# Performance work log

Hardware: AMD Instinct MI355X
Metric: run time of the kernel (lower is better)

## Reference

```python
import jax, jax.numpy as jnp
import numpy as np

EPS = 1e-6
H = 16       # query heads
KVH = 8      # kv heads
DH = 64      # head dim
HID = 1024


def _rms_norm(x, w, eps=EPS):
    ms = jnp.mean(jnp.square(x.astype(jnp.float32)), axis=-1, keepdims=True) + eps
    y = x.astype(jnp.float32) * jax.lax.rsqrt(ms)
    if w is not None:
        y = y * w.astype(jnp.float32)
    return y.astype(x.dtype)


def _rotate_half(x):
    h = x.shape[-1] // 2
    return jnp.concatenate([-x[..., h:], x[..., :h]], axis=-1)


def _multi_axis_rope(x, cos, sin, ndim):
    # x: [B,S,Hd,DH]; cos/sin: [S, rot_total]
    dh = x.shape[-1]
    rot = 2 * (dh // (2 * ndim))
    outs = []
    for i in range(ndim):
        sl = slice(i * rot, (i + 1) * rot)
        xp = x[..., sl]
        cp = cos[:, sl][:, None, :]   # [S,1,rot] broadcasts over heads
        sp = sin[:, sl][:, None, :]
        outs.append(xp * cp + _rotate_half(xp) * sp)
    return jnp.concatenate(outs, axis=-1)


def setup_inputs() -> dict:
    key = jax.random.key(0)
    ks = jax.random.split(key, 10)
    B, S = 4, 2048
    inp = {
        "hidden_states": jax.random.normal(ks[0], (B, S, HID), dtype=jnp.float32),
        "cos": jax.random.uniform(ks[1], (S, DH), dtype=jnp.float32, minval=-1.0, maxval=1.0),
        "sin": jax.random.uniform(ks[2], (S, DH), dtype=jnp.float32, minval=-1.0, maxval=1.0),
        "position_ids": jax.random.randint(ks[3], (B, S, 2), 0, 64).astype(jnp.int64),
        "attention_mask": jnp.ones((B, S), dtype=bool),
        "Wq": jax.random.normal(ks[4], (HID, H * DH), dtype=jnp.float32) * 0.02,
        "Wk": jax.random.normal(ks[5], (HID, KVH * DH), dtype=jnp.float32) * 0.02,
        "Wv": jax.random.normal(ks[6], (HID, KVH * DH), dtype=jnp.float32) * 0.02,
        "Wo": jax.random.normal(ks[7], (H * DH, HID), dtype=jnp.float32) * 0.02,
        "q_norm_w": jnp.ones((DH,), dtype=jnp.float32),
        "k_norm_w": jnp.ones((DH,), dtype=jnp.float32),
    }
    return inp


def reference(hidden_states, cos, sin, position_ids, attention_mask, Wq, Wk, Wv, Wo, q_norm_w, k_norm_w):
    B, S, _ = hidden_states.shape
    ndim = int(position_ids.shape[-1])

    q = (hidden_states @ Wq).reshape(B, S, H, DH)
    k = (hidden_states @ Wk).reshape(B, S, KVH, DH)
    v = (hidden_states @ Wv).reshape(B, S, KVH, DH)

    q = _rms_norm(q, q_norm_w)
    k = _rms_norm(k, k_norm_w)
    v = _rms_norm(v, None)  # v_norm has no scale

    q = _multi_axis_rope(q, cos, sin, ndim)
    k = _multi_axis_rope(k, cos, sin, ndim)

    # [B, heads, S, DH]; repeat kv heads for GQA
    q = q.transpose(0, 2, 1, 3)
    k = jnp.repeat(k.transpose(0, 2, 1, 3), H // KVH, axis=1)
    v = jnp.repeat(v.transpose(0, 2, 1, 3), H // KVH, axis=1)

    scores = jnp.einsum("bhqd,bhkd->bhqk", q, k)  # scaling = 1.0
    key_mask = attention_mask[:, None, None, :]
    scores = jnp.where(key_mask, scores, jnp.finfo(scores.dtype).min)
    probs = jax.nn.softmax(scores.astype(jnp.float32), axis=-1).astype(v.dtype)

    out = jnp.einsum("bhqk,bhkd->bhqd", probs, v)
    out = out.transpose(0, 2, 1, 3).reshape(B, S, H * DH)
    out = jnp.where(attention_mask[:, :, None], out, 0.0)
    return out @ Wo
```

## Files before the change

kernel.cpp:

```cpp
#include <hip/hip_runtime.h>
#include <stdint.h>
#include <stddef.h>

typedef unsigned short u16;
typedef unsigned int   u32;
typedef unsigned short u16x8 __attribute__((ext_vector_type(8)));
typedef __attribute__((ext_vector_type(8))) __bf16 bf16x8;
typedef __attribute__((ext_vector_type(4))) float f32x4;

__device__ __forceinline__ float bf2f(u16 v){
  union { unsigned u; float f; } x; x.u = ((unsigned)v) << 16; return x.f;
}
__device__ __forceinline__ u16 f2bf(float f){
  union { float f; unsigned u; } x; x.f = f;
  return (u16)((x.u + 0x7fffu + ((x.u >> 16) & 1u)) >> 16);
}

__device__ __forceinline__ float exp2_fast(float x){
  float r; asm("v_exp_f32 %0, %1" : "=v"(r) : "v"(x)); return r;
}
__device__ __forceinline__ u32 cvt_pk_bf16(float lo, float hi){
  u32 r; asm("v_cvt_pk_bf16_f32 %0, %1, %2" : "=v"(r) : "v"(lo), "v"(hi)); return r;
}

__device__ __forceinline__ f32x4 mfma16(bf16x8 a, bf16x8 b, f32x4 c){
  return __builtin_amdgcn_mfma_f32_16x16x32_bf16(a, b, c, 0, 0, 0);
}

#define AS1 __attribute__((address_space(1)))
#define AS3 __attribute__((address_space(3)))
__device__ __forceinline__ void gload_lds16(const void* g, void* l){
  __builtin_amdgcn_global_load_lds((const AS1 void*)g, (AS3 void*)l, 16, 0, 0);
}

__global__ void f32_to_bf16_swz(const float* __restrict__ in, u16* __restrict__ out,
                                int total_chunks){
  for (int i = blockIdx.x * blockDim.x + threadIdx.x; i < total_chunks;
       i += gridDim.x * blockDim.x){
    int row = i >> 7, c = i & 127;
    int cs = (c & ~7) | ((c & 7) ^ (row & 7));
    const float* p = in + ((size_t)i << 3);
    float4 v0 = *(const float4*)p;
    float4 v1 = *(const float4*)(p + 4);
    u16x8 o = { f2bf(v0.x), f2bf(v0.y), f2bf(v0.z), f2bf(v0.w),
                f2bf(v1.x), f2bf(v1.y), f2bf(v1.z), f2bf(v1.w) };
    *(u16x8*)(out + (((size_t)row << 7) + cs) * 8) = o;
  }
}

__global__ void conv_transpose_swz(const float* __restrict__ in, u16* __restrict__ out,
                                   int R, int C){
  __shared__ float t[32][33];
  int c0 = blockIdx.x * 32, r0 = blockIdx.y * 32;
  int tx = threadIdx.x, ty = threadIdx.y;
  t[ty][tx] = in[(size_t)(r0 + ty) * C + c0 + tx];
  __syncthreads();
  int tid = ty * 32 + tx;
  if (tid < 128){
    int orow = tid >> 2, oc = tid & 3;
    int gr = c0 + orow;
    int gc = (r0 >> 3) + oc;
    int gcs = (gc & ~7) | ((gc & 7) ^ (gr & 7));
    u16x8 v;
#pragma unroll
    for (int i = 0; i < 8; i++) v[i] = f2bf(t[oc * 8 + i][orow]);
    *(u16x8*)(out + (size_t)gr * R + gcs * 8) = v;
  }
}

template<int BM, int WM, bool F32OUT>
__global__ __launch_bounds__(512, 2)
void gemm256(const u16* __restrict__ A, const u16* __restrict__ Bt,
             void* __restrict__ Cv, int M, int N, int K){
  constexpr int MF = WM / 16;
  constexpr int ALOADS = BM / 64;
  __shared__ __align__(16) u16 Ab[3][BM * 64];
  const int tid = threadIdx.x;
  const int wid = tid >> 6, lane = tid & 63;
  const int g = lane >> 4, col = lane & 15;
  const int wm = wid >> 2, wn = wid & 3;
  const int swz = col & 7;

  int nb  = gridDim.x * gridDim.y;
  int lid = blockIdx.y * gridDim.x + blockIdx.x;
  int cpx = nb >> 3;
  int sid = (lid & 7) * cpx + (lid >> 3);
  int bx  = sid % gridDim.x, by = sid / gridDim.x;
  const int m0 = by * BM, n0 = bx * 256;

  f32x4 acc[MF][4];
#pragma unroll
  for (int i = 0; i < MF; i++)
#pragma unroll
    for (int j = 0; j < 4; j++) acc[i][j] = (f32x4){0.f, 0.f, 0.f, 0.f};

  const int arow = wid * 8 + (lane >> 3);
  const int acl  = (lane & 7) * 8;

  auto STAGE_A = [&](int bi, int k0){
#pragma unroll
    for (int j = 0; j < ALOADS; j++)
      gload_lds16(A + (size_t)(m0 + j * 64 + arow) * K + k0 + acl,
                  &Ab[bi][j * 4096 + wid * 512]);
  };

  const int NT = K >> 6;
  STAGE_A(0, 0);
  STAGE_A(1, 64);
  if (ALOADS == 4) asm volatile("s_waitcnt vmcnt(4)");
  else             asm volatile("s_waitcnt vmcnt(2)");
  __builtin_amdgcn_sched_barrier(0);
  __builtin_amdgcn_s_barrier();
  __builtin_amdgcn_sched_barrier(0);

  int cb = 0, sa = 2;
  for (int t = 0; t < NT; ++t){
    bf16x8 bfr[4][2];
#pragma unroll
    for (int ni = 0; ni < 4; ni++){
      const u16* bp = Bt + (size_t)(n0 + wn * 64 + ni * 16 + col) * K + t * 64;
#pragma unroll
      for (int ks = 0; ks < 2; ks++)
        bfr[ni][ks] = *(const bf16x8*)(bp + (((ks * 4 + g) ^ swz) << 3));
    }
    __builtin_amdgcn_sched_barrier(0);
    if (t + 2 < NT) STAGE_A(sa, (t + 2) * 64);
    __builtin_amdgcn_sched_barrier(0);

    const u16* Ac = &Ab[cb][0];
#pragma unroll
    for (int ph = 0; ph < MF / 4; ++ph){
      bf16x8 afr[4][2];
#pragma unroll
      for (int m2 = 0; m2 < 4; m2++){
        int row = wm * WM + (ph * 4 + m2) * 16 + col;
#pragma unroll
        for (int ks = 0; ks < 2; ks++)
          afr[m2][ks] = *(const bf16x8*)&Ac[row * 64 + (((ks * 4 + g) ^ swz) << 3)];
      }
      __builtin_amdgcn_s_setprio(1);
#pragma unroll
      for (int m2 = 0; m2 < 4; m2++)
#pragma unroll
        for (int ni = 0; ni < 4; ni++)
#pragma unroll
          for (int ks = 0; ks < 2; ks++)
            acc[ph * 4 + m2][ni] =
                mfma16(afr[m2][ks], bfr[ni][ks], acc[ph * 4 + m2][ni]);
      __builtin_amdgcn_s_setprio(0);
    }

    asm volatile("s_waitcnt lgkmcnt(0)");
    __builtin_amdgcn_sched_barrier(0);
    if (t + 2 < NT){
      if (ALOADS == 4) asm volatile("s_waitcnt vmcnt(4)");
      else             asm volatile("s_waitcnt vmcnt(2)");
    } else {
      asm volatile("s_waitcnt vmcnt(0)");
    }
    __builtin_amdgcn_sched_barrier(0);
    __builtin_amdgcn_s_barrier();
    __builtin_amdgcn_sched_barrier(0);
    cb = (cb == 2) ? 0 : cb + 1;
    sa = (sa == 2) ? 0 : sa + 1;
  }

#pragma unroll
  for (int mi = 0; mi < MF; mi++)
#pragma unroll
    for (int ni = 0; ni < 4; ni++)
#pragma unroll
      for (int r = 0; r < 4; r++){
        int row = m0 + wm * WM + mi * 16 + g * 4 + r;
        int cc  = n0 + wn * 64 + ni * 16 + col;
        if (F32OUT) ((float*)Cv)[(size_t)row * N + cc] = acc[mi][ni][r];
        else        ((u16*)Cv)[(size_t)row * N + cc] = f2bf(acc[mi][ni][r]);
      }
}

__global__ void prep_q(const u16* __restrict__ qkv, u16* __restrict__ Qn,
                       const float* __restrict__ cosb, const float* __restrict__ sinb,
                       const float* __restrict__ w){
  int gid = blockIdx.x * 4 + (threadIdx.x >> 6);
  int lane = threadIdx.x & 63;
  int s = gid & 2047;
  int bh = gid >> 11;
  int h = bh & 15, b = bh >> 4;
  float x = bf2f(qkv[((size_t)(b * 2048 + s)) * 2048 + h * 64 + lane]);
  float ss = x * x;
#pragma unroll
  for (int off = 32; off >= 1; off >>= 1) ss += __shfl_xor(ss, off, 64);
  float y = x * rsqrtf(ss * (1.f / 64.f) + 1e-6f);
  y *= w[lane];
  float yp = __shfl_xor(y, 16, 64);
  float rot = (lane & 16) ? yp : -yp;
  Qn[(size_t)gid * 64 + lane] = f2bf(y * cosb[s * 64 + lane] + rot * sinb[s * 64 + lane]);
}

__global__ void prep_k(const u16* __restrict__ qkv, u16* __restrict__ Kn,
                       const float* __restrict__ cosb, const float* __restrict__ sinb,
                       const float* __restrict__ w){
  int gid = blockIdx.x * 4 + (threadIdx.x >> 6);
  int lane = threadIdx.x & 63;
  int s = gid & 2047;
  int bk = gid >> 11;
  int kvh = bk & 7, b = bk >> 3;
  float x = bf2f(qkv[((size_t)(b * 2048 + s)) * 2048 + 1024 + kvh * 64 + lane]);
  float ss = x * x;
#pragma unroll
  for (int off = 32; off >= 1; off >>= 1) ss += __shfl_xor(ss, off, 64);
  float y = x * rsqrtf(ss * (1.f / 64.f) + 1e-6f);
  y *= w[lane];
  float yp = __shfl_xor(y, 16, 64);
  float rot = (lane & 16) ? yp : -yp;
  int swz = ((((lane >> 3) ^ s) & 7) << 3) | (lane & 7);
  Kn[(size_t)gid * 64 + swz] = f2bf(y * cosb[s * 64 + lane] + rot * sinb[s * 64 + lane]);
}

__global__ __launch_bounds__(256)
void prep_v(const u16* __restrict__ qkv, u16* __restrict__ Vn){
  int blk = blockIdx.x;
  int stile = blk & 31, kvh = (blk >> 5) & 7, b = blk >> 8;
  int wid = threadIdx.x >> 6, lane = threadIdx.x & 63;
  __shared__ u16 T[64][68];
#pragma unroll 4
  for (int j = 0; j < 16; j++){
    int sl = wid * 16 + j;
    int s = stile * 64 + sl;
    float x = bf2f(qkv[((size_t)(b * 2048 + s)) * 2048 + 1536 + kvh * 64 + lane]);
    float ss = x * x;
#pragma unroll
    for (int off = 32; off >= 1; off >>= 1) ss += __shfl_xor(ss, off, 64);
    T[sl][lane] = f2bf(x * rsqrtf(ss * (1.f / 64.f) + 1e-6f));
  }
  __syncthreads();
  size_t obase = ((size_t)(b * 8 + kvh) * 64) * 2048 + stile * 64;
#pragma unroll
  for (int it = 0; it < 2; it++){
    int t = it * 256 + threadIdx.x;
    int d = t >> 3, c = t & 7;
    int cl = c ^ (d & 7);
    u16x8 v;
#pragma unroll
    for (int i = 0; i < 8; i++) v[i] = T[cl * 8 + i][d];
    *(u16x8*)(Vn + obase + (size_t)d * 2048 + c * 8) = v;
  }
}

__global__ __launch_bounds__(256, 2)
void flash_attn(const u16* __restrict__ Qn, const u16* __restrict__ Kn,
                const u16* __restrict__ Vn, u16* __restrict__ AO){
  const int S = 2048;
  const float L2E = 1.4426950408889634f;
  const float C2 = 30.f;
  const int b = blockIdx.z, h = blockIdx.y, qt = blockIdx.x;
  const int kvh = h >> 1;
  const int wid = threadIdx.x >> 6, lane = threadIdx.x & 63;
  const int g = lane >> 4, col = lane & 15;
  const int q0 = qt * 256 + wid * 64;

  __shared__ __align__(16) u16 Klds[2][64 * 64];
  __shared__ __align__(16) u16 Vlds[2][64 * 64];
  __shared__ __align__(16) u16 Plds[4][16 * 64];

  bf16x8 ones;
#pragma unroll
  for (int i = 0; i < 8; i++) ones[i] = (__bf16)1.0f;

  bf16x8 aq[4][2];
#pragma unroll
  for (int cg = 0; cg < 4; cg++){
    const u16* qp = Qn + ((size_t)((b * 16 + h) * S) + q0 + cg * 16 + col) * 64;
    aq[cg][0] = *(const bf16x8*)(qp + g * 8);
    aq[cg][1] = *(const bf16x8*)(qp + 32 + g * 8);
  }

  const u16* Kbase = Kn + (size_t)(b * 8 + kvh) * S * 64;
  const u16* Vbase = Vn + (size_t)(b * 8 + kvh) * 64 * S;

  f32x4 acc[4][4];
  f32x4 lacc[4];
#pragma unroll
  for (int cg = 0; cg < 4; cg++){
    lacc[cg] = (f32x4){0.f, 0.f, 0.f, 0.f};
#pragma unroll
    for (int i = 0; i < 4; i++) acc[cg][i] = (f32x4){0.f, 0.f, 0.f, 0.f};
  }

  const int sw = col & 7;
  const int pswz = sw << 4;
  char* Pw = (char*)&Plds[wid][0];

  auto STAGE = [&](int bi, int kt){
    int kc0 = kt * 64;
#pragma unroll
    for (int cc = 0; cc < 2; cc++){
      int chunk = cc * 4 + wid;
      gload_lds16(Kbase + (size_t)kc0 * 64 + chunk * 512 + lane * 8,
                  &Klds[bi][chunk * 512]);
      int drow = chunk * 8 + (lane >> 3);
      gload_lds16(Vbase + (size_t)drow * S + kc0 + (lane & 7) * 8,
                  &Vlds[bi][chunk * 512]);
    }
  };

  int buf = 0;
  STAGE(0, 0);
  __syncthreads();

  for (int kt = 0; kt < S / 64; ++kt){
    if (kt + 1 < S / 64) STAGE(buf ^ 1, kt + 1);

    const u16* Kb = &Klds[buf][0];
    const u16* Vb = &Vlds[buf][0];

    bf16x8 kf[4][2], vf[4][2];
#pragma unroll
    for (int c = 0; c < 4; c++){
      const u16* kb = Kb + (c * 16 + col) * 64;
      kf[c][0] = *(const bf16x8*)(kb + (g ^ sw) * 8);
      kf[c][1] = *(const bf16x8*)(kb + ((4 + g) ^ sw) * 8);
      const u16* vb = Vb + (c * 16 + col) * 64;
      vf[c][0] = *(const bf16x8*)(vb + (g ^ sw) * 8);
      vf[c][1] = *(const bf16x8*)(vb + ((4 + g) ^ sw) * 8);
    }

#pragma unroll
    for (int cg = 0; cg < 4; cg++){
      f32x4 sf[4];
      __builtin_amdgcn_s_setprio(1);
#pragma unroll
      for (int c = 0; c < 4; c++){
        f32x4 z = (f32x4){0.f, 0.f, 0.f, 0.f};
        z = mfma16(kf[c][0], aq[cg][0], z);
        sf[c] = mfma16(kf[c][1], aq[cg][1], z);
      }
      __builtin_amdgcn_s_setprio(0);

#pragma unroll
      for (int c = 0; c < 4; c++){
        float p0 = exp2_fast(__builtin_fmaf(sf[c][0], L2E, -C2));
        float p1 = exp2_fast(__builtin_fmaf(sf[c][1], L2E, -C2));
        float p2 = exp2_fast(__builtin_fmaf(sf[c][2], L2E, -C2));
        float p3 = exp2_fast(__builtin_fmaf(sf[c][3], L2E, -C2));
        uint2 pw;
        pw.x = cvt_pk_bf16(p0, p1);
        pw.y = cvt_pk_bf16(p2, p3);
        *(uint2*)(Pw + ((col * 128 + c * 32 + g * 8) ^ pswz)) = pw;
      }

      bf16x8 pf0 = *(const bf16x8*)(Pw + ((col * 128 + g * 16) ^ pswz));
      bf16x8 pf1 = *(const bf16x8*)(Pw + ((col * 128 + 64 + g * 16) ^ pswz));
      __builtin_amdgcn_s_setprio(1);
#pragma unroll
      for (int cd = 0; cd < 4; cd++){
        acc[cg][cd] = mfma16(vf[cd][0], pf0, acc[cg][cd]);
        acc[cg][cd] = mfma16(vf[cd][1], pf1, acc[cg][cd]);
      }
      lacc[cg] = mfma16(ones, pf0, lacc[cg]);
      lacc[cg] = mfma16(ones, pf1, lacc[cg]);
      __builtin_amdgcn_s_setprio(0);
    }

    __syncthreads();
    buf ^= 1;
  }

#pragma unroll
  for (int cg = 0; cg < 4; cg++){
    float linv = 1.f / lacc[cg][0];
    int s = q0 + cg * 16 + col;
#pragma unroll
    for (int cd = 0; cd < 4; cd++){
      uint2 o;
      o.x = cvt_pk_bf16(acc[cg][cd][0] * linv, acc[cg][cd][1] * linv);
      o.y = cvt_pk_bf16(acc[cg][cd][2] * linv, acc[cg][cd][3] * linv);
      int pc = (cd * 2 + (g >> 1)) ^ sw;
      *(uint2*)(AO + (size_t)(b * S + s) * 1024 + h * 64 + pc * 8 + (g & 1) * 4) = o;
    }
  }
}

extern "C" void kernel_launch(void* const* d_in, const int* in_sizes, int n_in,
                              void* d_out, int out_size, void* d_ws, size_t ws_size,
                              hipStream_t stream){
  const int Btok = 8192;
  const float* hs   = (const float*)d_in[0];
  const float* cosb = (const float*)d_in[1];
  const float* sinb = (const float*)d_in[2];
  const float* Wq = (const float*)d_in[5];
  const float* Wk = (const float*)d_in[6];
  const float* Wv = (const float*)d_in[7];
  const float* Wo = (const float*)d_in[8];
  const float* qw = (const float*)d_in[9];
  const float* kw = (const float*)d_in[10];
  float* out = (float*)d_out;

  char* ws = (char*)d_ws;
  u16* hsB   = (u16*)ws;               ws += (size_t)Btok * 1024 * 2;
  u16* WqkvT = (u16*)ws;               ws += (size_t)2048 * 1024 * 2;
  u16* WoT   = (u16*)ws;               ws += (size_t)1024 * 1024 * 2;
  u16* QKV   = (u16*)ws;               ws += (size_t)Btok * 2048 * 2;
  u16* Qn    = (u16*)ws;               ws += (size_t)Btok * 1024 * 2;
  u16* Kn    = (u16*)ws;               ws += (size_t)Btok * 512  * 2;
  u16* Vn    = (u16*)ws;               ws += (size_t)Btok * 512  * 2;
  u16* AO    = hsB;

  f32_to_bf16_swz<<<2048, 256, 0, stream>>>(hs, hsB, Btok * 128);

  dim3 tb(32, 32);
  conv_transpose_swz<<<dim3(32, 32), tb, 0, stream>>>(Wq, WqkvT,               1024, 1024);
  conv_transpose_swz<<<dim3(16, 32), tb, 0, stream>>>(Wk, WqkvT + 1024 * 1024, 1024, 512);
  conv_transpose_swz<<<dim3(16, 32), tb, 0, stream>>>(Wv, WqkvT + 1536 * 1024, 1024, 512);
  conv_transpose_swz<<<dim3(32, 32), tb, 0, stream>>>(Wo, WoT,                 1024, 1024);

  gemm256<256, 128, false><<<dim3(8, 32), 512, 0, stream>>>(hsB, WqkvT, QKV, Btok, 2048, 1024);

  prep_q<<<32768, 256, 0, stream>>>(QKV, Qn, cosb, sinb, qw);
  prep_k<<<16384, 256, 0, stream>>>(QKV, Kn, cosb, sinb, kw);
  prep_v<<<1024, 256, 0, stream>>>(QKV, Vn);

  flash_attn<<<dim3(8, 16, 4), 256, 0, stream>>>(Qn, Kn, Vn, AO);

  gemm256<128, 64, true><<<dim3(4, 64), 512, 0, stream>>>(AO, WoT, out, Btok, 1024, 1024);
}
```

Baseline: 205.2 us.

## Fuse QKV RMSNorm, RoPE and layout into QKV GEMM epilogue

The separate prep_q, prep_k and prep_v kernels are removed. The QKV GEMM epilogue now computes per-row RMS norm with lane shuffles, applies the weights and RoPE from a packed cos/sin table, and writes Q, K (swizzled) and transposed V directly. This avoids writing and re-reading the intermediate QKV buffer and saves three launches. In exchange, the GEMM epilogue gains extra register pressure and uses scattered 2-byte stores for Q and K.

```diff
diff --git a/kernel.cpp b/kernel.cpp
--- a/kernel.cpp
+++ b/kernel.cpp
@@ -68,10 +68,19 @@
   }
 }
 
-template<int BM, int WM, bool F32OUT>
+__global__ void pack_cs(const float* __restrict__ cosb, const float* __restrict__ sinb,
+                        float2* __restrict__ cs, int n){
+  int i = blockIdx.x * 256 + threadIdx.x;
+  if (i < n) cs[i] = (float2){cosb[i], sinb[i]};
+}
+
+template<int BM, int WM, int EPI>
 __global__ __launch_bounds__(512, 2)
 void gemm256(const u16* __restrict__ A, const u16* __restrict__ Bt,
-             void* __restrict__ Cv, int M, int N, int K){
+             void* __restrict__ Cv, int M, int N, int K,
+             const float2* __restrict__ cs, const float* __restrict__ qw,
+             const float* __restrict__ kw, u16* __restrict__ Qn,
+             u16* __restrict__ Kn, u16* __restrict__ Vn){
   constexpr int MF = WM / 16;
   constexpr int ALOADS = BM / 64;
   __shared__ __align__(16) u16 Ab[3][BM * 64];
@@ -165,6 +174,92 @@
     sa = (sa == 2) ? 0 : sa + 1;
   }
 
+  if (EPI == 1){
+    const int colbase = n0 + wn * 64;
+    const int t0 = m0 + wm * WM;
+    const int bb = t0 >> 11;
+    if (colbase < 1536){
+      const bool isQ = colbase < 1024;
+      const int head = isQ ? (colbase >> 6) : ((colbase - 1024) >> 6);
+      const float* wp = isQ ? qw : kw;
+      float wv[4];
+#pragma unroll
+      for (int ni = 0; ni < 4; ni++) wv[ni] = wp[ni * 16 + col];
+      u16* outp = isQ ? Qn : Kn;
+      size_t hb = isQ ? ((size_t)(bb * 16 + head) * 2048)
+                      : ((size_t)(bb * 8 + head) * 2048);
+#pragma unroll
+      for (int mi = 0; mi < MF; mi++){
+        f32x4 ssv = (f32x4){0.f, 0.f, 0.f, 0.f};
+#pragma unroll
+        for (int ni = 0; ni < 4; ni++)
+#pragma unroll
+          for (int r = 0; r < 4; r++) ssv[r] += acc[mi][ni][r] * acc[mi][ni][r];
+#pragma unroll
+        for (int off = 1; off < 16; off <<= 1)
+#pragma unroll
+          for (int r = 0; r < 4; r++) ssv[r] += __shfl_xor(ssv[r], off, 64);
+        f32x4 rinv;
+#pragma unroll
+        for (int r = 0; r < 4; r++) rinv[r] = rsqrtf(ssv[r] * (1.f / 64.f) + 1e-6f);
+        int s0 = (t0 + mi * 16 + g * 4) & 2047;
+#pragma unroll
+        for (int np = 0; np < 2; np++){
+          int d0 = np * 32 + col, d1 = d0 + 16;
+#pragma unroll
+          for (int r = 0; r < 4; r++){
+            int s = s0 + r;
+            float y0 = acc[mi][np * 2][r]     * rinv[r] * wv[np * 2];
+            float y1 = acc[mi][np * 2 + 1][r] * rinv[r] * wv[np * 2 + 1];
+            float2 c0 = cs[s * 64 + d0];
+            float2 c1 = cs[s * 64 + d1];
+            float o0 = y0 * c0.x - y1 * c0.y;
+            float o1 = y1 * c1.x + y0 * c1.y;
+            if (isQ){
+              outp[(hb + s) * 64 + d0] = f2bf(o0);
+              outp[(hb + s) * 64 + d1] = f2bf(o1);
+            } else {
+              int z0 = ((((d0 >> 3) ^ s) & 7) << 3) | (d0 & 7);
+              int z1 = ((((d1 >> 3) ^ s) & 7) << 3) | (d1 & 7);
+              outp[(hb + s) * 64 + z0] = f2bf(o0);
+              outp[(hb + s) * 64 + z1] = f2bf(o1);
+            }
+          }
+        }
+      }
+    } else {
+      const int kvh = (colbase - 1536) >> 6;
+      const size_t vb0 = (size_t)(bb * 8 + kvh) * 64;
+#pragma unroll
+      for (int mi = 0; mi < MF; mi++){
+        f32x4 ssv = (f32x4){0.f, 0.f, 0.f, 0.f};
+#pragma unroll
+        for (int ni = 0; ni < 4; ni++)
+#pragma unroll
+          for (int r = 0; r < 4; r++) ssv[r] += acc[mi][ni][r] * acc[mi][ni][r];
+#pragma unroll
+        for (int off = 1; off < 16; off <<= 1)
+#pragma unroll
+          for (int r = 0; r < 4; r++) ssv[r] += __shfl_xor(ssv[r], off, 64);
+        f32x4 rinv;
+#pragma unroll
+        for (int r = 0; r < 4; r++) rinv[r] = rsqrtf(ssv[r] * (1.f / 64.f) + 1e-6f);
+        int s0 = (t0 + mi * 16 + g * 4) & 2047;
+#pragma unroll
+        for (int ni = 0; ni < 4; ni++){
+          int d = ni * 16 + col;
+          uint2 o;
+          o.x = cvt_pk_bf16(acc[mi][ni][0] * rinv[0], acc[mi][ni][1] * rinv[1]);
+          o.y = cvt_pk_bf16(acc[mi][ni][2] * rinv[2], acc[mi][ni][3] * rinv[3]);
+          size_t addr = (vb0 + d) * 2048 + (s0 & ~63)
+                      + ((((s0 >> 3) ^ (d & 7)) & 7) << 3) + (s0 & 7);
+          *(uint2*)(Vn + addr) = o;
+        }
+      }
+    }
+    return;
+  }
+
 #pragma unroll
   for (int mi = 0; mi < MF; mi++)
 #pragma unroll
@@ -173,78 +268,9 @@
       for (int r = 0; r < 4; r++){
         int row = m0 + wm * WM + mi * 16 + g * 4 + r;
         int cc  = n0 + wn * 64 + ni * 16 + col;
-        if (F32OUT) ((float*)Cv)[(size_t)row * N + cc] = acc[mi][ni][r];
-        else        ((u16*)Cv)[(size_t)row * N + cc] = f2bf(acc[mi][ni][r]);
-      }
-}
-
-__global__ void prep_q(const u16* __restrict__ qkv, u16* __restrict__ Qn,
-                       const float* __restrict__ cosb, const float* __restrict__ sinb,
-                       const float* __restrict__ w){
-  int gid = blockIdx.x * 4 + (threadIdx.x >> 6);
-  int lane = threadIdx.x & 63;
-  int s = gid & 2047;
-  int bh = gid >> 11;
-  int h = bh & 15, b = bh >> 4;
-  float x = bf2f(qkv[((size_t)(b * 2048 + s)) * 2048 + h * 64 + lane]);
-  float ss = x * x;
-#pragma unroll
-  for (int off = 32; off >= 1; off >>= 1) ss += __shfl_xor(ss, off, 64);
-  float y = x * rsqrtf(ss * (1.f / 64.f) + 1e-6f);
-  y *= w[lane];
-  float yp = __shfl_xor(y, 16, 64);
-  float rot = (lane & 16) ? yp : -yp;
-  Qn[(size_t)gid * 64 + lane] = f2bf(y * cosb[s * 64 + lane] + rot * sinb[s * 64 + lane]);
-}
-
-__global__ void prep_k(const u16* __restrict__ qkv, u16* __restrict__ Kn,
-                       const float* __restrict__ cosb, const float* __restrict__ sinb,
-                       const float* __restrict__ w){
-  int gid = blockIdx.x * 4 + (threadIdx.x >> 6);
-  int lane = threadIdx.x & 63;
-  int s = gid & 2047;
-  int bk = gid >> 11;
-  int kvh = bk & 7, b = bk >> 3;
-  float x = bf2f(qkv[((size_t)(b * 2048 + s)) * 2048 + 1024 + kvh * 64 + lane]);
-  float ss = x * x;
-#pragma unroll
-  for (int off = 32; off >= 1; off >>= 1) ss += __shfl_xor(ss, off, 64);
-  float y = x * rsqrtf(ss * (1.f / 64.f) + 1e-6f);
-  y *= w[lane];
-  float yp = __shfl_xor(y, 16, 64);
-  float rot = (lane & 16) ? yp : -yp;
-  int swz = ((((lane >> 3) ^ s) & 7) << 3) | (lane & 7);
-  Kn[(size_t)gid * 64 + swz] = f2bf(y * cosb[s * 64 + lane] + rot * sinb[s * 64 + lane]);
-}
-
-__global__ __launch_bounds__(256)
-void prep_v(const u16* __restrict__ qkv, u16* __restrict__ Vn){
-  int blk = blockIdx.x;
-  int stile = blk & 31, kvh = (blk >> 5) & 7, b = blk >> 8;
-  int wid = threadIdx.x >> 6, lane = threadIdx.x & 63;
-  __shared__ u16 T[64][68];
-#pragma unroll 4
-  for (int j = 0; j < 16; j++){
-    int sl = wid * 16 + j;
-    int s = stile * 64 + sl;
-    float x = bf2f(qkv[((size_t)(b * 2048 + s)) * 2048 + 1536 + kvh * 64 + lane]);
-    float ss = x * x;
-#pragma unroll
-    for (int off = 32; off >= 1; off >>= 1) ss += __shfl_xor(ss, off, 64);
-    T[sl][lane] = f2bf(x * rsqrtf(ss * (1.f / 64.f) + 1e-6f));
-  }
-  __syncthreads();
-  size_t obase = ((size_t)(b * 8 + kvh) * 64) * 2048 + stile * 64;
-#pragma unroll
-  for (int it = 0; it < 2; it++){
-    int t = it * 256 + threadIdx.x;
-    int d = t >> 3, c = t & 7;
-    int cl = c ^ (d & 7);
-    u16x8 v;
-#pragma unroll
-    for (int i = 0; i < 8; i++) v[i] = T[cl * 8 + i][d];
-    *(u16x8*)(Vn + obase + (size_t)d * 2048 + c * 8) = v;
-  }
+        if (EPI == 2) ((float*)Cv)[(size_t)row * N + cc] = acc[mi][ni][r];
+        else          ((u16*)Cv)[(size_t)row * N + cc] = f2bf(acc[mi][ni][r]);
+      }
 }
 
 __global__ __launch_bounds__(256, 2)
@@ -400,10 +426,10 @@
   u16* hsB   = (u16*)ws;               ws += (size_t)Btok * 1024 * 2;
   u16* WqkvT = (u16*)ws;               ws += (size_t)2048 * 1024 * 2;
   u16* WoT   = (u16*)ws;               ws += (size_t)1024 * 1024 * 2;
-  u16* QKV   = (u16*)ws;               ws += (size_t)Btok * 2048 * 2;
   u16* Qn    = (u16*)ws;               ws += (size_t)Btok * 1024 * 2;
   u16* Kn    = (u16*)ws;               ws += (size_t)Btok * 512  * 2;
   u16* Vn    = (u16*)ws;               ws += (size_t)Btok * 512  * 2;
+  float2* cst = (float2*)ws;           ws += (size_t)2048 * 64 * 8;
   u16* AO    = hsB;
 
   f32_to_bf16_swz<<<2048, 256, 0, stream>>>(hs, hsB, Btok * 128);
@@ -413,14 +439,14 @@
   conv_transpose_swz<<<dim3(16, 32), tb, 0, stream>>>(Wk, WqkvT + 1024 * 1024, 1024, 512);
   conv_transpose_swz<<<dim3(16, 32), tb, 0, stream>>>(Wv, WqkvT + 1536 * 1024, 1024, 512);
   conv_transpose_swz<<<dim3(32, 32), tb, 0, stream>>>(Wo, WoT,                 1024, 1024);
-
-  gemm256<256, 128, false><<<dim3(8, 32), 512, 0, stream>>>(hsB, WqkvT, QKV, Btok, 2048, 1024);
-
-  prep_q<<<32768, 256, 0, stream>>>(QKV, Qn, cosb, sinb, qw);
-  prep_k<<<16384, 256, 0, stream>>>(QKV, Kn, cosb, sinb, kw);
-  prep_v<<<1024, 256, 0, stream>>>(QKV, Vn);
+  pack_cs<<<512, 256, 0, stream>>>(cosb, sinb, cst, 2048 * 64);
+
+  gemm256<256, 128, 1><<<dim3(8, 32), 512, 0, stream>>>(
+      hsB, WqkvT, nullptr, Btok, 2048, 1024, cst, qw, kw, Qn, Kn, Vn);
 
   flash_attn<<<dim3(8, 16, 4), 256, 0, stream>>>(Qn, Kn, Vn, AO);
 
-  gemm256<128, 64, true><<<dim3(4, 64), 512, 0, stream>>>(AO, WoT, out, Btok, 1024, 1024);
-}
+  gemm256<128, 64, 2><<<dim3(4, 64), 512, 0, stream>>>(
+      AO, WoT, out, Btok, 1024, 1024, nullptr, nullptr, nullptr,
+      nullptr, nullptr, nullptr);
+}
```

Result: faster. 185.6 us (-9.6%).
